# Optimization experiments

Hardware: AMD Instinct MI355X
Metric: run time of the kernel (lower is better)

## Reference

```python
import jax, jax.numpy as jnp
import numpy as np

N = 8192
IN_DIM = 512
OUT_DIM = 256
ALPHA = 0.2  # LeakyReLU negative slope


def setup_inputs() -> dict:
    key = jax.random.key(0)
    k_nodes, k_edge, k_W, k_Wb, k_a1, k_a1b, k_a2, k_a2b = jax.random.split(key, 8)
    nodes = jax.random.normal(k_nodes, (N, IN_DIM), dtype=jnp.float32)
    edge_mat = jax.random.uniform(k_edge, (N, N)) > 0.5
    edge_mat = edge_mat | jnp.eye(N, dtype=bool)
    s_W = 1.0 / np.sqrt(IN_DIM)
    s_a = 1.0 / np.sqrt(OUT_DIM)
    W_w = jax.random.uniform(k_W, (OUT_DIM, IN_DIM), minval=-s_W, maxval=s_W, dtype=jnp.float32)
    W_b = jax.random.uniform(k_Wb, (OUT_DIM,), minval=-s_W, maxval=s_W, dtype=jnp.float32)
    a1_w = jax.random.uniform(k_a1, (1, OUT_DIM), minval=-s_a, maxval=s_a, dtype=jnp.float32)
    a1_b = jax.random.uniform(k_a1b, (1,), minval=-s_a, maxval=s_a, dtype=jnp.float32)
    a2_w = jax.random.uniform(k_a2, (1, OUT_DIM), minval=-s_a, maxval=s_a, dtype=jnp.float32)
    a2_b = jax.random.uniform(k_a2b, (1,), minval=-s_a, maxval=s_a, dtype=jnp.float32)
    return {"nodes": nodes, "edge_mat": edge_mat, "W_w": W_w, "W_b": W_b,
            "a1_w": a1_w, "a1_b": a1_b, "a2_w": a2_w, "a2_b": a2_b}


def reference(nodes, edge_mat, W_w, W_b, a1_w, a1_b, a2_w, a2_b):
    Wh = nodes @ W_w.T + W_b                      # [N, OUT_DIM]
    Wh1 = Wh @ a1_w.T + a1_b                      # [N, 1]
    Wh2 = Wh @ a2_w.T + a2_b                      # [N, 1]
    scores = jax.nn.leaky_relu(Wh1 + Wh2.T, negative_slope=ALPHA)  # [N, N]
    masked = jnp.where(edge_mat, scores, -jnp.inf)
    attention = jax.nn.softmax(masked, axis=1)    # [N, N]
    return attention @ Wh                         # [N, OUT_DIM]
```

## Files before the change

kernel.cpp:

```cpp
#include <hip/hip_runtime.h>
#include <hip/hip_bf16.h>
#include <stdint.h>


#define NN 8192
#define IND 512
#define OUTD 256

typedef __attribute__((ext_vector_type(8))) short short8;
typedef __attribute__((ext_vector_type(4))) short short4v;
typedef __attribute__((ext_vector_type(4))) float f32x4;
typedef __attribute__((ext_vector_type(4))) unsigned int u32x4;

#define AS_GLOBAL __attribute__((address_space(1)))
#define AS_LDS __attribute__((address_space(3)))

static __device__ __forceinline__ short f2bf(float f) {
  return __builtin_bit_cast(short, __float2bfloat16(f));
}

extern "C" __global__ __launch_bounds__(256) void k_convert_w(
    const float* __restrict__ W, short* __restrict__ W2) {
  const int t = blockIdx.x * 256 + threadIdx.x;
  const int row = t >> 6, kb = t & 63;
  const float* src = W + row * IND + kb * 8;
  f32x4 x0 = *(const f32x4*)src;
  f32x4 x1 = *(const f32x4*)(src + 4);
  short8 o;
  o[0] = f2bf(x0[0]); o[1] = f2bf(x0[1]); o[2] = f2bf(x0[2]); o[3] = f2bf(x0[3]);
  o[4] = f2bf(x1[0]); o[5] = f2bf(x1[1]); o[6] = f2bf(x1[2]); o[7] = f2bf(x1[3]);
  *(short8*)(W2 + (size_t)kb * 2048 + row * 8) = o;
}

extern "C" __global__ __launch_bounds__(128) void k_wh(
    const float* __restrict__ nodes, const short* __restrict__ W2,
    const float* __restrict__ Wb, const float* __restrict__ a1w,
    const float* __restrict__ a1b, const float* __restrict__ a2w,
    const float* __restrict__ a2b, short* __restrict__ WhL,
    float* __restrict__ s1, float* __restrict__ s2) {
  const int tid = threadIdx.x;
  const int wv = tid >> 6, lane = tid & 63, g = lane >> 4, m = lane & 15;
  const int rowbase = blockIdx.x * 32 + wv * 16;

  f32x4 acc[16];
#pragma unroll
  for (int nf = 0; nf < 16; ++nf) acc[nf] = (f32x4){0.f, 0.f, 0.f, 0.f};

  const float* arow = nodes + (size_t)(rowbase + m) * IND;
  const short* bb = W2 + (size_t)g * 2048 + m * 8;
#pragma unroll 4
  for (int k0 = 0; k0 < IND; k0 += 32) {
    const float* ap = arow + k0 + g * 8;
    f32x4 x0 = *(const f32x4*)ap;
    f32x4 x1 = *(const f32x4*)(ap + 4);
    short8 af;
    af[0] = f2bf(x0[0]); af[1] = f2bf(x0[1]); af[2] = f2bf(x0[2]); af[3] = f2bf(x0[3]);
    af[4] = f2bf(x1[0]); af[5] = f2bf(x1[1]); af[6] = f2bf(x1[2]); af[7] = f2bf(x1[3]);
    const short* bk = bb + (size_t)(k0 >> 3) * 2048;
#pragma unroll
    for (int nf = 0; nf < 16; ++nf) {
      short8 bf = *(const short8*)(bk + nf * 128);
      acc[nf] = __builtin_amdgcn_mfma_f32_16x16x32_bf16(af, bf, acc[nf], 0, 0, 0);
    }
  }

  float p1[4] = {0.f, 0.f, 0.f, 0.f}, p2[4] = {0.f, 0.f, 0.f, 0.f};
#pragma unroll
  for (int nf = 0; nf < 16; ++nf) {
    const int n = nf * 16 + m;
    const float b = Wb[n], c1 = a1w[n], c2 = a2w[n];
#pragma unroll
    for (int r = 0; r < 4; ++r) {
      float v = acc[nf][r] + b;
      acc[nf][r] = v;
      p1[r] += c1 * v;
      p2[r] += c2 * v;
    }
  }
#pragma unroll
  for (int off = 1; off < 16; off <<= 1) {
#pragma unroll
    for (int r = 0; r < 4; ++r) {
      p1[r] += __shfl_xor(p1[r], off);
      p2[r] += __shfl_xor(p2[r], off);
    }
  }
  if (m == 0) {
    const float b1 = a1b[0], b2 = a2b[0];
#pragma unroll
    for (int r = 0; r < 4; ++r) {
      const int row = rowbase + g * 4 + r;
      s1[row] = p1[r] + b1;
      s2[row] = p2[r] + b2;
    }
  }

  const size_t cbase = ((size_t)(rowbase >> 3) + (g >> 1)) * 2048 + (g & 1) * 4;
#pragma unroll
  for (int nf = 0; nf < 16; ++nf) {
    short4v o;
#pragma unroll
    for (int r = 0; r < 4; ++r) o[r] = f2bf(acc[nf][r]);
    *(short4v*)(WhL + cbase + (size_t)(nf * 16 + m) * 8) = o;
  }
}

extern "C" __global__ __launch_bounds__(256) void k_prep(
    const float* __restrict__ s1, const float* __restrict__ s2,
    float* __restrict__ sAC, uint32_t* __restrict__ sPK) {
  const int i = blockIdx.x * 256 + threadIdx.x;
  const float v1 = s1[i], v2 = s2[i];
  sAC[i] = __expf(v1);
  sAC[NN + i] = __expf(0.2f * v1);
  const float B = __expf(v2), D = __expf(0.2f * v2);
  sPK[2 * i] = __builtin_bit_cast(uint32_t, B);
  sPK[2 * i + 1] =
      ((uint32_t)(uint16_t)f2bf(D) << 16) | (uint16_t)(uint16_t)f2bf(v2);
}

extern "C" __global__ __launch_bounds__(256) void k_mask(
    const int* __restrict__ mask, uint32_t* __restrict__ bm) {
  const int tid = threadIdx.x;
  const int wv = tid >> 6, lane = tid & 63;
  const int gw = blockIdx.x * 4 + wv;
  const size_t base = (size_t)gw * 16384;
#pragma unroll 4
  for (int it = 0; it < 64; ++it) {
    const size_t ib = base + (size_t)it * 256;
    unsigned long long b0 = __ballot(mask[ib + lane] != 0);
    unsigned long long b1 = __ballot(mask[ib + 64 + lane] != 0);
    unsigned long long b2 = __ballot(mask[ib + 128 + lane] != 0);
    unsigned long long b3 = __ballot(mask[ib + 192 + lane] != 0);
    if (lane < 8) {
      unsigned long long s01 = (lane & 2) ? b1 : b0;
      unsigned long long s23 = (lane & 2) ? b3 : b2;
      unsigned long long sel = (lane & 4) ? s23 : s01;
      bm[ib / 32 + lane] = (uint32_t)(sel >> ((lane & 1) * 32));
    }
  }
}

extern "C" __global__ __launch_bounds__(512, 4) void k_attn(
    const uint32_t* __restrict__ bm, const short* __restrict__ WhL,
    const float* __restrict__ s1, const float* __restrict__ sAC,
    const uint32_t* __restrict__ sPK,
    float* __restrict__ pnum, float* __restrict__ pden) {
  __shared__ char smem[73728];
  uint32_t* PKs = (uint32_t*)(smem + 49152);
  uint32_t* BMs = (uint32_t*)(smem + 57344);

  const int tid = threadIdx.x;
  const int w = tid >> 6, lane = tid & 63, g = lane >> 4, m = lane & 15;
  const int rt = blockIdx.x >> 3, jc = blockIdx.x & 7;
  const int rg = w & 3, ns = w >> 2;
  const int rb = rt * 128 + rg * 32;

  const float T0 = -s1[rb + m],        T1 = -s1[rb + 16 + m];
  const float A0 = sAC[rb + m],        A1 = sAC[rb + 16 + m];
  const float C0 = sAC[NN + rb + m],   C1 = sAC[NN + rb + 16 + m];

  f32x4 acc0[8], acc1[8];
#pragma unroll
  for (int nf = 0; nf < 8; ++nf) {
    acc0[nf] = (f32x4){0.f, 0.f, 0.f, 0.f};
    acc1[nf] = (f32x4){0.f, 0.f, 0.f, 0.f};
  }
  float den0 = 0.f, den1 = 0.f;

  {
    const int rloc = tid >> 2, wq = (tid & 3) * 8;
    const uint32_t* src = bm + (size_t)(rt * 128 + rloc) * 256 + jc * 32 + wq;
    u32x4 a = *(const u32x4*)src;
    u32x4 b = *(const u32x4*)(src + 4);
#pragma unroll
    for (int i = 0; i < 4; ++i)
      BMs[rloc * 32 + ((wq + i) ^ (rloc & 31))] = a[i];
#pragma unroll
    for (int i = 0; i < 4; ++i)
      BMs[rloc * 32 + ((wq + 4 + i) ^ (rloc & 31))] = b[i];
  }
  __builtin_amdgcn_global_load_lds(
      (const AS_GLOBAL void*)((const char*)sPK + (size_t)jc * 8192 +
                              w * 1024 + lane * 16),
      (AS_LDS void*)(smem + 49152 + w * 1024), 16, 0, 0);
  const short* gS = WhL + (size_t)jc * 262144;
#pragma unroll
  for (int s = 0; s < 2; ++s) {
#pragma unroll
    for (int c = 0; c < 2; ++c) {
      __builtin_amdgcn_global_load_lds(
          (const AS_GLOBAL void*)(gS + s * 8192 + w * 1024 + c * 512 + lane * 8),
          (AS_LDS void*)(smem + s * 16384 + w * 2048 + c * 1024), 16, 0, 0);
    }
  }
  __syncthreads();

  auto build = [&](float T, float A, float C, uint32_t mbits,
                   const u32x4& q0, const u32x4& q1,
                   const u32x4& q2, const u32x4& q3, float& den) -> short8 {
    const uint32_t Bv[8] = {q0[0], q0[2], q1[0], q1[2],
                            q2[0], q2[2], q3[0], q3[2]};
    const uint32_t Dv[8] = {q0[1], q0[3], q1[1], q1[3],
                            q2[1], q2[3], q3[1], q3[3]};
    short8 af;
#pragma unroll
    for (int i = 0; i < 8; ++i) {
      const float s2v = __builtin_bit_cast(float, Dv[i] << 16);
      const bool pos = s2v > T;
      const float wv = __builtin_bit_cast(float, pos ? Bv[i] : (Dv[i] & 0xFFFF0000u));
      const float a = pos ? A : C;
      const float val = wv * a;
      const float pv = ((mbits >> i) & 1u) ? val : 0.f;
      den += pv;
      af[i] = f2bf(pv);
    }
    return af;
  };

  for (int u = 0; u < 32; ++u) {
    asm volatile("s_waitcnt vmcnt(2)" ::: "memory");
    __builtin_amdgcn_s_barrier();
    __builtin_amdgcn_sched_barrier(0);

    {
      const int up = (u + 2 < 32) ? (u + 2) : 31;
      const int bi = (u + 2) % 3;
      const short* gn = gS + up * 8192 + w * 1024 + lane * 8;
      char* ldb = smem + bi * 16384 + w * 2048;
      __builtin_amdgcn_global_load_lds((const AS_GLOBAL void*)gn,
                                       (AS_LDS void*)ldb, 16, 0, 0);
      __builtin_amdgcn_global_load_lds((const AS_GLOBAL void*)(gn + 512),
                                       (AS_LDS void*)(ldb + 1024), 16, 0, 0);
    }

    const uint32_t cw0 = BMs[(rg * 32 + m) * 32 + (u ^ m)];
    const uint32_t cw1 = BMs[(rg * 32 + 16 + m) * 32 + (u ^ (16 + m))];
    const uint32_t* pk = &PKs[u * 64 + g * 16];
    const u32x4 q0 = *(const u32x4*)(pk + 0);
    const u32x4 q1 = *(const u32x4*)(pk + 4);
    const u32x4 q2 = *(const u32x4*)(pk + 8);
    const u32x4 q3 = *(const u32x4*)(pk + 12);
    short8 af0 = build(T0, A0, C0, cw0 >> (g * 8), q0, q1, q2, q3, den0);
    short8 af1 = build(T1, A1, C1, cw1 >> (g * 8), q0, q1, q2, q3, den1);

    const short* bl = (const short*)(smem + (u % 3) * 16384) +
                      g * 2048 + (ns * 128 + m) * 8;
#pragma unroll
    for (int nf = 0; nf < 8; ++nf) {
      short8 bf = *(const short8*)(bl + nf * 128);
      acc0[nf] = __builtin_amdgcn_mfma_f32_16x16x32_bf16(af0, bf, acc0[nf], 0, 0, 0);
      acc1[nf] = __builtin_amdgcn_mfma_f32_16x16x32_bf16(af1, bf, acc1[nf], 0, 0, 0);
    }
  }

  den0 += __shfl_xor(den0, 16); den0 += __shfl_xor(den0, 32);
  den1 += __shfl_xor(den1, 16); den1 += __shfl_xor(den1, 32);
  if (ns == 0 && lane < 16) {
    pden[jc * NN + rb + m] = den0;
    pden[jc * NN + rb + 16 + m] = den1;
  }

  float* pn = pnum + (size_t)jc * NN * OUTD + (size_t)rb * OUTD + ns * 128;
#pragma unroll
  for (int r = 0; r < 4; ++r) {
    const int q = g * 4 + r;
#pragma unroll
    for (int nf = 0; nf < 8; ++nf) {
      pn[(size_t)q * OUTD + nf * 16 + m] = acc0[nf][r];
      pn[(size_t)(16 + q) * OUTD + nf * 16 + m] = acc1[nf][r];
    }
  }
}

extern "C" __global__ __launch_bounds__(256) void k_comb(
    const float* __restrict__ pnum, const float* __restrict__ pden,
    float* __restrict__ out) {
  const int idx = blockIdx.x * 256 + threadIdx.x;
  const int row = idx >> 6, c4 = (idx & 63) * 4;
  f32x4 s = (f32x4){0.f, 0.f, 0.f, 0.f};
  float d = 0.f;
#pragma unroll
  for (int jc = 0; jc < 8; ++jc) {
    f32x4 v = *(const f32x4*)(pnum + ((size_t)jc * NN + row) * OUTD + c4);
    s += v;
    d += pden[jc * NN + row];
  }
  const float inv = 1.f / d;
  *(f32x4*)(out + (size_t)row * OUTD + c4) = s * inv;
}

extern "C" void kernel_launch(void* const* d_in, const int* in_sizes, int n_in,
                              void* d_out, int out_size, void* d_ws, size_t ws_size,
                              hipStream_t stream) {
  const float* nodes = (const float*)d_in[0];
  const int*   mask  = (const int*)d_in[1];
  const float* W_w   = (const float*)d_in[2];
  const float* W_b   = (const float*)d_in[3];
  const float* a1w   = (const float*)d_in[4];
  const float* a1b   = (const float*)d_in[5];
  const float* a2w   = (const float*)d_in[6];
  const float* a2b   = (const float*)d_in[7];
  float* out = (float*)d_out;

  char* ws = (char*)d_ws;
  short*    WhL  = (short*)(ws);
  float*    s1   = (float*)(ws + (size_t)4  * 1024 * 1024);
  float*    s2   = (float*)(ws + (size_t)4  * 1024 * 1024 + 32768);
  short*    W2   = (short*)(ws + (size_t)4  * 1024 * 1024 + 65536);
  uint32_t* bmp  = (uint32_t*)(ws + (size_t)5  * 1024 * 1024);
  float*    sAC  = (float*)(ws + (size_t)13 * 1024 * 1024);
  uint32_t* sPK  = (uint32_t*)(ws + (size_t)14 * 1024 * 1024);
  float*    pnum = (float*)(ws + (size_t)16 * 1024 * 1024);
  float*    pden = (float*)(ws + (size_t)96 * 1024 * 1024);

  hipLaunchKernelGGL(k_mask, dim3(1024), dim3(256), 0, stream, mask, bmp);
  hipLaunchKernelGGL(k_convert_w, dim3(64), dim3(256), 0, stream, W_w, W2);
  hipLaunchKernelGGL(k_wh, dim3(256), dim3(128), 0, stream,
                     nodes, W2, W_b, a1w, a1b, a2w, a2b, WhL, s1, s2);
  hipLaunchKernelGGL(k_prep, dim3(32), dim3(256), 0, stream, s1, s2, sAC, sPK);
  hipLaunchKernelGGL(k_attn, dim3(512), dim3(512), 0, stream,
                     bmp, WhL, s1, sAC, sPK, pnum, pden);
  hipLaunchKernelGGL(k_comb, dim3(2048), dim3(256), 0, stream,
                     pnum, pden, out);
}
```

Baseline: 175.4 us.

## Merge mask packing, Wh projection and score prep into one heterogeneous launch

Combines the mask bit-packing kernel, the Wh GEMM kernel and the exp-prep kernel into a single launch. Blocks are interleaved so one in nine does the projection (now 64 rows per 256-thread block) and the rest pack the mask. The exp/packing of scores is computed directly in the GEMM epilogue, which removes the s2 buffer and a separate launch. This is meant to cut launch overhead and overlap the bandwidth-bound mask conversion with the compute-bound GEMM, at the cost of higher register pressure from the shared launch bounds and possible imbalance between the two block types.

```diff
diff --git a/kernel.cpp b/kernel.cpp
--- a/kernel.cpp
+++ b/kernel.cpp
@@ -32,15 +32,42 @@
   *(short8*)(W2 + (size_t)kb * 2048 + row * 8) = o;
 }
 
-extern "C" __global__ __launch_bounds__(128) void k_wh(
+extern "C" __global__ __launch_bounds__(256, 2) void k_front(
+    const int* __restrict__ mask, uint32_t* __restrict__ bm,
     const float* __restrict__ nodes, const short* __restrict__ W2,
     const float* __restrict__ Wb, const float* __restrict__ a1w,
     const float* __restrict__ a1b, const float* __restrict__ a2w,
     const float* __restrict__ a2b, short* __restrict__ WhL,
-    float* __restrict__ s1, float* __restrict__ s2) {
+    float* __restrict__ s1, float* __restrict__ sAC,
+    uint32_t* __restrict__ sPK) {
+  const int bid = blockIdx.x;
   const int tid = threadIdx.x;
-  const int wv = tid >> 6, lane = tid & 63, g = lane >> 4, m = lane & 15;
-  const int rowbase = blockIdx.x * 32 + wv * 16;
+  const int wv = tid >> 6, lane = tid & 63;
+
+  if (bid % 9 != 8) {
+    const int mb = (bid / 9) * 8 + (bid % 9);
+    const int gw = mb * 4 + wv;
+    const size_t base = (size_t)gw * 16384;
+#pragma unroll 4
+    for (int it = 0; it < 64; ++it) {
+      const size_t ib = base + (size_t)it * 256;
+      unsigned long long b0 = __ballot(mask[ib + lane] != 0);
+      unsigned long long b1 = __ballot(mask[ib + 64 + lane] != 0);
+      unsigned long long b2 = __ballot(mask[ib + 128 + lane] != 0);
+      unsigned long long b3 = __ballot(mask[ib + 192 + lane] != 0);
+      if (lane < 8) {
+        unsigned long long s01 = (lane & 2) ? b1 : b0;
+        unsigned long long s23 = (lane & 2) ? b3 : b2;
+        unsigned long long sel = (lane & 4) ? s23 : s01;
+        bm[ib / 32 + lane] = (uint32_t)(sel >> ((lane & 1) * 32));
+      }
+    }
+    return;
+  }
+
+  const int wb = bid / 9;
+  const int g = lane >> 4, m = lane & 15;
+  const int rowbase = wb * 64 + wv * 16;
 
   f32x4 acc[16];
 #pragma unroll
@@ -90,8 +117,14 @@
 #pragma unroll
     for (int r = 0; r < 4; ++r) {
       const int row = rowbase + g * 4 + r;
-      s1[row] = p1[r] + b1;
-      s2[row] = p2[r] + b2;
+      const float v1 = p1[r] + b1, v2 = p2[r] + b2;
+      s1[row] = v1;
+      sAC[row] = __expf(v1);
+      sAC[NN + row] = __expf(0.2f * v1);
+      const float B = __expf(v2), D = __expf(0.2f * v2);
+      sPK[2 * row] = __builtin_bit_cast(uint32_t, B);
+      sPK[2 * row + 1] =
+          ((uint32_t)(uint16_t)f2bf(D) << 16) | (uint16_t)f2bf(v2);
     }
   }
 
@@ -102,41 +135,6 @@
 #pragma unroll
     for (int r = 0; r < 4; ++r) o[r] = f2bf(acc[nf][r]);
     *(short4v*)(WhL + cbase + (size_t)(nf * 16 + m) * 8) = o;
-  }
-}
-
-extern "C" __global__ __launch_bounds__(256) void k_prep(
-    const float* __restrict__ s1, const float* __restrict__ s2,
-    float* __restrict__ sAC, uint32_t* __restrict__ sPK) {
-  const int i = blockIdx.x * 256 + threadIdx.x;
-  const float v1 = s1[i], v2 = s2[i];
-  sAC[i] = __expf(v1);
-  sAC[NN + i] = __expf(0.2f * v1);
-  const float B = __expf(v2), D = __expf(0.2f * v2);
-  sPK[2 * i] = __builtin_bit_cast(uint32_t, B);
-  sPK[2 * i + 1] =
-      ((uint32_t)(uint16_t)f2bf(D) << 16) | (uint16_t)(uint16_t)f2bf(v2);
-}
-
-extern "C" __global__ __launch_bounds__(256) void k_mask(
-    const int* __restrict__ mask, uint32_t* __restrict__ bm) {
-  const int tid = threadIdx.x;
-  const int wv = tid >> 6, lane = tid & 63;
-  const int gw = blockIdx.x * 4 + wv;
-  const size_t base = (size_t)gw * 16384;
-#pragma unroll 4
-  for (int it = 0; it < 64; ++it) {
-    const size_t ib = base + (size_t)it * 256;
-    unsigned long long b0 = __ballot(mask[ib + lane] != 0);
-    unsigned long long b1 = __ballot(mask[ib + 64 + lane] != 0);
-    unsigned long long b2 = __ballot(mask[ib + 128 + lane] != 0);
-    unsigned long long b3 = __ballot(mask[ib + 192 + lane] != 0);
-    if (lane < 8) {
-      unsigned long long s01 = (lane & 2) ? b1 : b0;
-      unsigned long long s23 = (lane & 2) ? b3 : b2;
-      unsigned long long sel = (lane & 4) ? s23 : s01;
-      bm[ib / 32 + lane] = (uint32_t)(sel >> ((lane & 1) * 32));
-    }
   }
 }
 
@@ -305,7 +303,6 @@
   char* ws = (char*)d_ws;
   short*    WhL  = (short*)(ws);
   float*    s1   = (float*)(ws + (size_t)4  * 1024 * 1024);
-  float*    s2   = (float*)(ws + (size_t)4  * 1024 * 1024 + 32768);
   short*    W2   = (short*)(ws + (size_t)4  * 1024 * 1024 + 65536);
   uint32_t* bmp  = (uint32_t*)(ws + (size_t)5  * 1024 * 1024);
   float*    sAC  = (float*)(ws + (size_t)13 * 1024 * 1024);
@@ -313,11 +310,10 @@
   float*    pnum = (float*)(ws + (size_t)16 * 1024 * 1024);
   float*    pden = (float*)(ws + (size_t)96 * 1024 * 1024);
 
-  hipLaunchKernelGGL(k_mask, dim3(1024), dim3(256), 0, stream, mask, bmp);
   hipLaunchKernelGGL(k_convert_w, dim3(64), dim3(256), 0, stream, W_w, W2);
-  hipLaunchKernelGGL(k_wh, dim3(256), dim3(128), 0, stream,
-                     nodes, W2, W_b, a1w, a1b, a2w, a2b, WhL, s1, s2);
-  hipLaunchKernelGGL(k_prep, dim3(32), dim3(256), 0, stream, s1, s2, sAC, sPK);
+  hipLaunchKernelGGL(k_front, dim3(1152), dim3(256), 0, stream,
+                     mask, bmp, nodes, W2, W_b, a1w, a1b, a2w, a2b,
+                     WhL, s1, sAC, sPK);
   hipLaunchKernelGGL(k_attn, dim3(512), dim3(512), 0, stream,
                      bmp, WhL, s1, sAC, sPK, pnum, pden);
   hipLaunchKernelGGL(k_comb, dim3(2048), dim3(256), 0, stream,
```

After: 176.5 us. No clear change (+0.6%).
